# Kernel tuning notes

Measured on AMD Instinct MI355X. Metric: run time of the kernel, lower is better.

The kernel has to match this reference:

```python
import jax, jax.numpy as jnp
import numpy as np

D_MODEL = 1024
N_HEAD = 16
D_HEAD = 64  # scale uses d_head even though heads are never split in this module
HD = N_HEAD * D_HEAD  # 1024
LN_EPS = 1e-5


def setup_inputs() -> dict:
    key = jax.random.key(0)
    ks = jax.random.split(key, 12)
    B, S = 8, 2048
    s = 0.02
    return {
        "q": jax.random.normal(ks[0], (B, S, D_MODEL), jnp.float32),
        "k": jax.random.normal(ks[1], (B, S, D_MODEL), jnp.float32),
        "v": jax.random.normal(ks[2], (B, S, D_MODEL), jnp.float32),
        "Wq": jax.random.normal(ks[3], (HD, D_MODEL), jnp.float32) * s,
        "Wk": jax.random.normal(ks[4], (HD, D_MODEL), jnp.float32) * s,
        "bk": jax.random.normal(ks[5], (HD,), jnp.float32) * s,
        "Wv": jax.random.normal(ks[6], (HD, D_MODEL), jnp.float32) * s,
        "bv": jax.random.normal(ks[7], (HD,), jnp.float32) * s,
        "Wo": jax.random.normal(ks[8], (D_MODEL, HD), jnp.float32) * s,
        "bo": jax.random.normal(ks[9], (D_MODEL,), jnp.float32) * s,
        "gamma": jnp.ones((D_MODEL,), jnp.float32),
        "beta": jnp.zeros((D_MODEL,), jnp.float32),
    }


def reference(q, k, v, Wq, Wk, bk, Wv, bv, Wo, bo, gamma, beta):
    scale = 1.0 / np.sqrt(D_HEAD).astype(np.float32)
    # projections (q_head has no bias, matching nn.Linear(bias=False))
    qh = jnp.einsum('bsm,hm->bsh', q, Wq) * scale      # [B,S,HD]
    kh = jnp.einsum('bsm,hm->bsh', k, Wk) + bk         # [B,S,HD]
    vh = jnp.einsum('bsm,hm->bsh', v, Wv) + bv         # [B,S,HD]
    # single effective head: full HD contraction (heads never split in source)
    scores = jnp.einsum('bid,bjd->bij', qh, kh)        # [B,Sq,Sk]
    dtype = scores.dtype
    probs = jax.nn.softmax(scores.astype(jnp.float32), axis=-1).astype(dtype)
    attn = jnp.einsum('bij,bjd->bid', probs, vh)       # [B,Sq,HD]
    attn_out = jnp.einsum('bsh,mh->bsm', attn, Wo) + bo
    x = q + attn_out                                   # dropout/drop_path = identity at eval
    mu = jnp.mean(x, axis=-1, keepdims=True)
    var = jnp.mean(jnp.square(x - mu), axis=-1, keepdims=True)
    return (x - mu) * jax.lax.rsqrt(var + LN_EPS) * gamma + beta
```

## Files before the change

kernel.cpp:

```cpp
#include <hip/hip_runtime.h>

typedef unsigned short u16;
typedef __attribute__((ext_vector_type(8))) short bf16x8;
typedef __attribute__((ext_vector_type(4))) float f32x4;

#define DEVINL static __device__ __forceinline__

DEVINL u16 f2bf(float x) {
  unsigned u = __float_as_uint(x);
  unsigned r = (u + 0x7FFFu + ((u >> 16) & 1u)) >> 16;
  return (u16)r;
}
DEVINL float bf2f(u16 h) { return __uint_as_float(((unsigned)h) << 16); }

DEVINL void gload_lds16(const u16* g, u16* l) {
  __builtin_amdgcn_global_load_lds(
      (const __attribute__((address_space(1))) void*)g,
      (__attribute__((address_space(3))) void*)l, 16, 0, 0);
}

DEVINL void stage_half(const u16* gbase, int K, u16* ldst, int tid) {
#pragma unroll
  for (int i = 0; i < 2; i++) {
    int q = i * 512 + tid;
    int r = q >> 2, gl = (q & 3) ^ ((q >> 4) & 3);
    gload_lds16(gbase + (size_t)r * K + gl * 8, ldst + q * 8);
  }
}

template <bool HAS_BIAS, bool RESID, bool OUT_F32>
__global__ __launch_bounds__(512, 2) void gemm_bt(
    const u16* __restrict__ Ap, const u16* __restrict__ Bp,
    const float* __restrict__ bias, const float* __restrict__ resid,
    void* __restrict__ Cp, int N, int K, long long Az, long long Bz,
    long long Cz, float scale) {
  const int gx = gridDim.x, gy = gridDim.y;
  int lin = blockIdx.x + gx * (blockIdx.y + gy * blockIdx.z);
  const int nwg = gx * gy * gridDim.z;
  if ((nwg & 7) == 0) {
    const int chunk = nwg >> 3;
    lin = (lin & 7) * chunk + (lin >> 3);
  }
  const int bz = lin / (gx * gy);
  const int rem = lin - bz * gx * gy;
  const int m0 = (rem / gx) * 256, n0 = (rem % gx) * 256;

  const int tid = threadIdx.x, lane = tid & 63, wv = tid >> 6;
  const int wr = wv >> 2, wc = wv & 3, lr = lane & 15, lh = lane >> 4;

  __shared__ u16 lds[3 * 16384];

  const u16* A = Ap + (size_t)bz * Az + (size_t)m0 * K;
  const u16* B = Bp + (size_t)bz * Bz + (size_t)n0 * K;

  f32x4 acc[8][4] = {};
  const int nt = K >> 5;

  stage_half(A, K, &lds[0], tid);
  stage_half(B, K, &lds[8192], tid);
  stage_half(A + 32, K, &lds[16384], tid);
  stage_half(B + 32, K, &lds[16384 + 8192], tid);
  asm volatile("s_waitcnt vmcnt(4)" ::: "memory");
  __builtin_amdgcn_s_barrier();

  int d = 0;
  for (int t = 0; t < nt; ++t) {
    const u16* la = &lds[d * 16384];
    const u16* lb = la + 8192;
    int dn = d + 2;
    if (dn >= 3) dn -= 3;
    const bool doPre = (t + 2) < nt;

    bf16x8 bfv[4], af[4];
#pragma unroll
    for (int n = 0; n < 4; n++) {
      int row = wc * 64 + n * 16 + lr;
      bfv[n] = *(const bf16x8*)&lb[row * 32 + (lh ^ ((row >> 2) & 3)) * 8];
    }
#pragma unroll
    for (int m = 0; m < 4; m++) {
      int row = wr * 128 + m * 16 + lr;
      af[m] = *(const bf16x8*)&la[row * 32 + (lh ^ ((row >> 2) & 3)) * 8];
    }
    if (doPre) stage_half(A + (size_t)(t + 2) * 32, K, &lds[dn * 16384], tid);
    __builtin_amdgcn_s_setprio(1);
#pragma unroll
    for (int m = 0; m < 4; m++)
#pragma unroll
      for (int n = 0; n < 4; n++)
        acc[m][n] = __builtin_amdgcn_mfma_f32_16x16x32_bf16(af[m], bfv[n],
                                                            acc[m][n], 0, 0, 0);
    __builtin_amdgcn_s_setprio(0);

#pragma unroll
    for (int m = 0; m < 4; m++) {
      int row = wr * 128 + (m + 4) * 16 + lr;
      af[m] = *(const bf16x8*)&la[row * 32 + (lh ^ ((row >> 2) & 3)) * 8];
    }
    if (doPre)
      stage_half(B + (size_t)(t + 2) * 32, K, &lds[dn * 16384 + 8192], tid);
    __builtin_amdgcn_s_setprio(1);
#pragma unroll
    for (int m = 0; m < 4; m++)
#pragma unroll
      for (int n = 0; n < 4; n++)
        acc[m + 4][n] = __builtin_amdgcn_mfma_f32_16x16x32_bf16(
            af[m], bfv[n], acc[m + 4][n], 0, 0, 0);
    __builtin_amdgcn_s_setprio(0);

    if (t + 2 < nt)
      asm volatile("s_waitcnt vmcnt(4)" ::: "memory");
    else if (t + 1 < nt)
      asm volatile("s_waitcnt vmcnt(0)" ::: "memory");
    if (t + 1 < nt) __builtin_amdgcn_s_barrier();
    if (++d == 3) d = 0;
  }

  float* Cf = nullptr;
  u16* Ch = nullptr;
  if constexpr (OUT_F32)
    Cf = (float*)Cp + (size_t)bz * Cz;
  else
    Ch = (u16*)Cp + (size_t)bz * Cz;
#pragma unroll
  for (int m = 0; m < 8; m++) {
#pragma unroll
    for (int j = 0; j < 4; j++) {
      int row = m0 + wr * 128 + m * 16 + lh * 4 + j;
#pragma unroll
      for (int n = 0; n < 4; n++) {
        int col = n0 + wc * 64 + n * 16 + lr;
        float val = acc[m][n][j] * scale;
        if constexpr (HAS_BIAS) val += bias[col];
        if constexpr (RESID) val += resid[(size_t)row * N + col];
        if constexpr (OUT_F32)
          Cf[(size_t)row * N + col] = val;
        else
          Ch[(size_t)row * N + col] = f2bf(val);
      }
    }
  }
}

__global__ __launch_bounds__(256) void cvt8(const float* __restrict__ in,
                                            u16* __restrict__ out) {
  const size_t i = ((size_t)blockIdx.x * 256 + threadIdx.x) * 8;
  f32x4 a = *(const f32x4*)&in[i];
  f32x4 b = *(const f32x4*)&in[i + 4];
  bf16x8 h;
#pragma unroll
  for (int u = 0; u < 4; u++) h[u] = (short)f2bf(a[u]);
#pragma unroll
  for (int u = 0; u < 4; u++) h[4 + u] = (short)f2bf(b[u]);
  *(bf16x8*)&out[i] = h;
}

__global__ __launch_bounds__(256) void transpose_bf16(const u16* __restrict__ in,
                                                      u16* __restrict__ out,
                                                      int R, int C) {
  const int z = blockIdx.z;
  const u16* I = in + (size_t)z * R * C;
  u16* O = out + (size_t)z * R * C;
  __shared__ u16 t[64][72];
  const int r0 = blockIdx.y * 64, c0 = blockIdx.x * 64;
  const int tid = threadIdx.x;
#pragma unroll
  for (int i = 0; i < 2; i++) {
    int e = (i * 256 + tid) * 8;
    int r = e >> 6, c = e & 63;
    bf16x8 v = *(const bf16x8*)&I[(size_t)(r0 + r) * C + c0 + c];
#pragma unroll
    for (int u = 0; u < 8; u++) t[r][c + u] = (u16)v[u];
  }
  __syncthreads();
#pragma unroll
  for (int i = 0; i < 2; i++) {
    int e = (i * 256 + tid) * 8;
    int orow = e >> 6, oc = e & 63;
    bf16x8 v;
#pragma unroll
    for (int u = 0; u < 8; u++) v[u] = (short)t[oc + u][orow];
    *(bf16x8*)&O[(size_t)(c0 + orow) * R + r0 + oc] = v;
  }
}

__global__ __launch_bounds__(256) void softmax_rows(u16* __restrict__ p) {
  const size_t base = (size_t)blockIdx.x * 2048;
  const int tid = threadIdx.x, lane = tid & 63, wv = tid >> 6;
  bf16x8 v = *(const bf16x8*)&p[base + tid * 8];
  float f[8];
#pragma unroll
  for (int u = 0; u < 8; u++) f[u] = bf2f((u16)v[u]);
  float mx = f[0];
#pragma unroll
  for (int u = 1; u < 8; u++) mx = fmaxf(mx, f[u]);
#pragma unroll
  for (int o = 32; o; o >>= 1) mx = fmaxf(mx, __shfl_xor(mx, o, 64));
  __shared__ float rm[4], rs[4];
  if (lane == 0) rm[wv] = mx;
  __syncthreads();
  mx = fmaxf(fmaxf(rm[0], rm[1]), fmaxf(rm[2], rm[3]));
  float s = 0.f, e[8];
#pragma unroll
  for (int u = 0; u < 8; u++) {
    e[u] = __expf(f[u] - mx);
    s += e[u];
  }
#pragma unroll
  for (int o = 32; o; o >>= 1) s += __shfl_xor(s, o, 64);
  if (lane == 0) rs[wv] = s;
  __syncthreads();
  s = rs[0] + rs[1] + rs[2] + rs[3];
  float inv = 1.f / s;
  bf16x8 o8;
#pragma unroll
  for (int u = 0; u < 8; u++) o8[u] = (short)f2bf(e[u] * inv);
  *(bf16x8*)&p[base + tid * 8] = o8;
}

__global__ __launch_bounds__(256) void ln_rows(const float* __restrict__ x,
                                               const float* __restrict__ gamma,
                                               const float* __restrict__ beta,
                                               float* __restrict__ out) {
  const size_t base = (size_t)blockIdx.x * 1024;
  const int tid = threadIdx.x, lane = tid & 63, wv = tid >> 6;
  f32x4 v = *(const f32x4*)&x[base + tid * 4];
  float s = v[0] + v[1] + v[2] + v[3];
  float q = v[0] * v[0] + v[1] * v[1] + v[2] * v[2] + v[3] * v[3];
#pragma unroll
  for (int o = 32; o; o >>= 1) {
    s += __shfl_xor(s, o, 64);
    q += __shfl_xor(q, o, 64);
  }
  __shared__ float rs[4], rq[4];
  if (lane == 0) {
    rs[wv] = s;
    rq[wv] = q;
  }
  __syncthreads();
  s = rs[0] + rs[1] + rs[2] + rs[3];
  q = rq[0] + rq[1] + rq[2] + rq[3];
  float mean = s * (1.f / 1024.f);
  float var = q * (1.f / 1024.f) - mean * mean;
  float rstd = rsqrtf(var + 1e-5f);
  f32x4 g = *(const f32x4*)&gamma[tid * 4];
  f32x4 b = *(const f32x4*)&beta[tid * 4];
  f32x4 o;
#pragma unroll
  for (int u = 0; u < 4; u++) o[u] = (v[u] - mean) * rstd * g[u] + b[u];
  *(f32x4*)&out[base + tid * 4] = o;
}

extern "C" void kernel_launch(void* const* d_in, const int* in_sizes, int n_in,
                              void* d_out, int out_size, void* d_ws,
                              size_t ws_size, hipStream_t stream) {
  (void)in_sizes; (void)n_in; (void)out_size; (void)ws_size;
  const float* q = (const float*)d_in[0];
  const float* k = (const float*)d_in[1];
  const float* v = (const float*)d_in[2];
  const float* Wq = (const float*)d_in[3];
  const float* Wk = (const float*)d_in[4];
  const float* bk = (const float*)d_in[5];
  const float* Wv = (const float*)d_in[6];
  const float* bv = (const float*)d_in[7];
  const float* Wo = (const float*)d_in[8];
  const float* bo = (const float*)d_in[9];
  const float* gamma = (const float*)d_in[10];
  const float* beta = (const float*)d_in[11];
  float* out = (float*)d_out;

  char* ws = (char*)d_ws;
  const size_t SZ_QKV = (size_t)16384 * 1024 * 2;
  u16* qh = (u16*)(ws);
  u16* kh = (u16*)(ws + SZ_QKV);
  u16* vh = (u16*)(ws + 2 * SZ_QKV);
  u16* vhT = (u16*)(ws + 3 * SZ_QKV);
  u16* probs = (u16*)(ws + 4 * SZ_QKV);
  u16* qkvb = probs;
  float* xbuf = (float*)(ws + 4 * SZ_QKV);
  u16* attn = qh;
  u16* Wqb = (u16*)(ws + 4 * SZ_QKV + (size_t)67108864);
  u16* Wkb = Wqb + 1048576;
  u16* Wvb = Wkb + 1048576;
  u16* Wob = Wvb + 1048576;

  cvt8<<<512, 256, 0, stream>>>(Wq, Wqb);
  cvt8<<<512, 256, 0, stream>>>(Wk, Wkb);
  cvt8<<<512, 256, 0, stream>>>(Wv, Wvb);
  cvt8<<<512, 256, 0, stream>>>(Wo, Wob);

  dim3 gp(4, 64, 1);
  cvt8<<<8192, 256, 0, stream>>>(q, qkvb);
  gemm_bt<false, false, false><<<gp, 512, 0, stream>>>(
      qkvb, Wqb, nullptr, nullptr, qh, 1024, 1024, 0, 0, 0, 0.125f);
  cvt8<<<8192, 256, 0, stream>>>(k, qkvb);
  gemm_bt<true, false, false><<<gp, 512, 0, stream>>>(
      qkvb, Wkb, bk, nullptr, kh, 1024, 1024, 0, 0, 0, 1.0f);
  cvt8<<<8192, 256, 0, stream>>>(v, qkvb);
  gemm_bt<true, false, false><<<gp, 512, 0, stream>>>(
      qkvb, Wvb, bv, nullptr, vh, 1024, 1024, 0, 0, 0, 1.0f);

  transpose_bf16<<<dim3(16, 32, 8), 256, 0, stream>>>(vh, vhT, 2048, 1024);

  gemm_bt<false, false, false><<<dim3(8, 8, 8), 512, 0, stream>>>(
      qh, kh, nullptr, nullptr, probs, 2048, 1024, 2097152LL, 2097152LL,
      4194304LL, 1.0f);

  softmax_rows<<<16384, 256, 0, stream>>>(probs);

  gemm_bt<false, false, false><<<dim3(4, 8, 8), 512, 0, stream>>>(
      probs, vhT, nullptr, nullptr, attn, 1024, 2048, 4194304LL, 2097152LL,
      2097152LL, 1.0f);

  gemm_bt<true, true, true><<<dim3(4, 64, 1), 512, 0, stream>>>(
      attn, Wob, bo, q, xbuf, 1024, 1024, 0, 0, 0, 1.0f);

  ln_rows<<<16384, 256, 0, stream>>>(xbuf, gamma, beta, out);
}
```

Before: 437.0 us.

## Restructure GEMM main loop to K=64 tiles with double-buffered LDS and phased barriers

The bf16 GEMM mainloop is rewritten to stage 64-wide K slices, with a new 8-way XOR swizzle, into two LDS buffers in place of 32-wide slices in a triple buffer. Each iteration is split into four phases, and each phase issues barriers around its MFMA cluster. The prefetch of A and B for the next tile is spread across these phases. The aim is fewer loop iterations and barriers per unit of K, plus more MFMA work per LDS load. In exchange, LDS use grows to 128KB per block and barriers increase inside an iteration, which may reduce occupancy from the launch bound of 2 blocks per CU.

```diff
diff --git a/kernel.cpp b/kernel.cpp
--- a/kernel.cpp
+++ b/kernel.cpp
@@ -19,12 +19,13 @@
       (__attribute__((address_space(3))) void*)l, 16, 0, 0);
 }
 
-DEVINL void stage_half(const u16* gbase, int K, u16* ldst, int tid) {
-#pragma unroll
-  for (int i = 0; i < 2; i++) {
-    int q = i * 512 + tid;
-    int r = q >> 2, gl = (q & 3) ^ ((q >> 4) & 3);
-    gload_lds16(gbase + (size_t)r * K + gl * 8, ldst + q * 8);
+DEVINL void stage64(const u16* gbase, int K, u16* ldst, int tid) {
+#pragma unroll
+  for (int i = 0; i < 4; i++) {
+    int g = i * 512 + tid;
+    int r = g >> 3;
+    int ks = (g & 7) ^ (r & 7);
+    gload_lds16(gbase + (size_t)r * K + ks * 8, ldst + g * 8);
   }
 }
 
@@ -48,72 +49,70 @@
   const int tid = threadIdx.x, lane = tid & 63, wv = tid >> 6;
   const int wr = wv >> 2, wc = wv & 3, lr = lane & 15, lh = lane >> 4;
 
-  __shared__ u16 lds[3 * 16384];
+  __shared__ u16 lds[65536];
 
   const u16* A = Ap + (size_t)bz * Az + (size_t)m0 * K;
   const u16* B = Bp + (size_t)bz * Bz + (size_t)n0 * K;
 
   f32x4 acc[8][4] = {};
-  const int nt = K >> 5;
-
-  stage_half(A, K, &lds[0], tid);
-  stage_half(B, K, &lds[8192], tid);
-  stage_half(A + 32, K, &lds[16384], tid);
-  stage_half(B + 32, K, &lds[16384 + 8192], tid);
-  asm volatile("s_waitcnt vmcnt(4)" ::: "memory");
+  const int nt = K >> 6;
+
+  stage64(A, K, &lds[0], tid);
+  stage64(B, K, &lds[16384], tid);
+  asm volatile("s_waitcnt vmcnt(0)" ::: "memory");
   __builtin_amdgcn_s_barrier();
 
-  int d = 0;
-  for (int t = 0; t < nt; ++t) {
-    const u16* la = &lds[d * 16384];
-    const u16* lb = la + 8192;
-    int dn = d + 2;
-    if (dn >= 3) dn -= 3;
-    const bool doPre = (t + 2) < nt;
-
-    bf16x8 bfv[4], af[4];
-#pragma unroll
-    for (int n = 0; n < 4; n++) {
-      int row = wc * 64 + n * 16 + lr;
-      bfv[n] = *(const bf16x8*)&lb[row * 32 + (lh ^ ((row >> 2) & 3)) * 8];
+  for (int T = 0; T < nt; ++T) {
+    u16* bufA = &lds[(T & 1) * 32768];
+    u16* bufB = bufA + 16384;
+    u16* nbufA = &lds[((T + 1) & 1) * 32768];
+    u16* nbufB = nbufA + 16384;
+    const bool pre = (T + 1) < nt;
+    bf16x8 bf[4][2];
+
+#pragma unroll
+    for (int p = 0; p < 4; ++p) {
+      bf16x8 af[2][2];
+#pragma unroll
+      for (int i = 0; i < 2; ++i) {
+        int r = wr * 128 + (2 * p + i) * 16 + lr;
+#pragma unroll
+        for (int h = 0; h < 2; ++h)
+          af[i][h] =
+              *(const bf16x8*)&bufA[(r * 8 + (((h << 2) | lh) ^ (r & 7))) * 8];
+      }
+      if (p == 0) {
+#pragma unroll
+        for (int n = 0; n < 4; ++n) {
+          int r = wc * 64 + n * 16 + lr;
+#pragma unroll
+          for (int h = 0; h < 2; ++h)
+            bf[n][h] =
+                *(const bf16x8*)&bufB[(r * 8 + (((h << 2) | lh) ^ (r & 7))) * 8];
+        }
+        if (pre) stage64(A + (size_t)(T + 1) * 64, K, nbufA, tid);
+        asm volatile("s_waitcnt lgkmcnt(8)" ::: "memory");
+      }
+      if (p == 1 && pre) stage64(B + (size_t)(T + 1) * 64, K, nbufB, tid);
+
+      __builtin_amdgcn_s_barrier();
+      asm volatile("s_waitcnt lgkmcnt(0)" ::: "memory");
+      __builtin_amdgcn_sched_barrier(0);
+
+      __builtin_amdgcn_s_setprio(1);
+#pragma unroll
+      for (int i = 0; i < 2; ++i)
+#pragma unroll
+        for (int n = 0; n < 4; ++n)
+#pragma unroll
+          for (int h = 0; h < 2; ++h)
+            acc[2 * p + i][n] = __builtin_amdgcn_mfma_f32_16x16x32_bf16(
+                af[i][h], bf[n][h], acc[2 * p + i][n], 0, 0, 0);
+      __builtin_amdgcn_s_setprio(0);
+
+      if (p == 3 && pre) asm volatile("s_waitcnt vmcnt(0)" ::: "memory");
+      if (!(p == 3 && !pre)) __builtin_amdgcn_s_barrier();
     }
-#pragma unroll
-    for (int m = 0; m < 4; m++) {
-      int row = wr * 128 + m * 16 + lr;
-      af[m] = *(const bf16x8*)&la[row * 32 + (lh ^ ((row >> 2) & 3)) * 8];
-    }
-    if (doPre) stage_half(A + (size_t)(t + 2) * 32, K, &lds[dn * 16384], tid);
-    __builtin_amdgcn_s_setprio(1);
-#pragma unroll
-    for (int m = 0; m < 4; m++)
-#pragma unroll
-      for (int n = 0; n < 4; n++)
-        acc[m][n] = __builtin_amdgcn_mfma_f32_16x16x32_bf16(af[m], bfv[n],
-                                                            acc[m][n], 0, 0, 0);
-    __builtin_amdgcn_s_setprio(0);
-
-#pragma unroll
-    for (int m = 0; m < 4; m++) {
-      int row = wr * 128 + (m + 4) * 16 + lr;
-      af[m] = *(const bf16x8*)&la[row * 32 + (lh ^ ((row >> 2) & 3)) * 8];
-    }
-    if (doPre)
-      stage_half(B + (size_t)(t + 2) * 32, K, &lds[dn * 16384 + 8192], tid);
-    __builtin_amdgcn_s_setprio(1);
-#pragma unroll
-    for (int m = 0; m < 4; m++)
-#pragma unroll
-      for (int n = 0; n < 4; n++)
-        acc[m + 4][n] = __builtin_amdgcn_mfma_f32_16x16x32_bf16(
-            af[m], bfv[n], acc[m + 4][n], 0, 0, 0);
-    __builtin_amdgcn_s_setprio(0);
-
-    if (t + 2 < nt)
-      asm volatile("s_waitcnt vmcnt(4)" ::: "memory");
-    else if (t + 1 < nt)
-      asm volatile("s_waitcnt vmcnt(0)" ::: "memory");
-    if (t + 1 < nt) __builtin_amdgcn_s_barrier();
-    if (++d == 3) d = 0;
   }
 
   float* Cf = nullptr;
```

Result: no change. 428.9 us (-1.9%).
